# Kernel tuning notes

Measured on AMD Instinct MI355X. Metric: run time of the kernel, lower is better.

The kernel has to match this reference:

```python
import jax, jax.numpy as jnp
import numpy as np
from jax import lax

B, L, D, F = 32, 512, 256, 256
K = 3
EPS = 1e-5


def _layer_norm(h, g, b):
    mu = jnp.mean(h, axis=-1, keepdims=True)
    var = jnp.var(h, axis=-1, keepdims=True)
    return (h - mu) * lax.rsqrt(var + EPS) * g + b


def _conv1d(h, w, b):
    # h: [B, L, Cin], w: [K, Cin, Cout] -> [B, L, Cout], 'same' padding (pad=1, k=3)
    return lax.conv_general_dilated(h, w, window_strides=(1,), padding=[(1, 1)],
                                    dimension_numbers=('NWC', 'WIO', 'NWC')) + b


def _duration_predictor(x, c1w, c1b, ln1g, ln1b, c2w, c2b, ln2g, ln2b, lw, lb):
    h = jax.nn.relu(_layer_norm(_conv1d(x, c1w, c1b), ln1g, ln1b))
    h = jax.nn.relu(_layer_norm(_conv1d(h, c2w, c2b), ln2g, ln2b))
    d = jax.nn.relu(h @ lw + lb)  # [B, L, 1]
    return d[..., 0]              # [B, L] (squeeze, training mode)


def _expand_one(xb, dur, M):
    # xb: [L, D], dur: [L] int. Repeat row i dur[i] times, zero-pad to M frames.
    cs = jnp.cumsum(dur)                              # [L]
    t = jnp.arange(M)                                 # [M]
    idx = jnp.searchsorted(cs, t, side='right')       # phoneme id per frame
    valid = t < cs[-1]
    out = jnp.take(xb, jnp.clip(idx, 0, xb.shape[0] - 1), axis=0)
    return jnp.where(valid[:, None], out, jnp.zeros((), xb.dtype))


def setup_inputs() -> dict:
    key = jax.random.key(0)
    ks = jax.random.split(key, 8)
    s_c = 1.0 / np.sqrt(K * F)
    s_l = 1.0 / np.sqrt(F)
    return {
        'x': jax.random.normal(ks[0], (B, L, D), jnp.float32),
        'durations': jax.random.randint(ks[1], (B, L), 0, 7),
        'mel_max_length': 4096,
        'conv1_w': jax.random.normal(ks[2], (K, D, F), jnp.float32) * s_c,
        'conv1_b': jnp.zeros((F,), jnp.float32),
        'ln1_g': jnp.ones((F,), jnp.float32),
        'ln1_b': jnp.zeros((F,), jnp.float32),
        'conv2_w': jax.random.normal(ks[3], (K, F, F), jnp.float32) * s_c,
        'conv2_b': jnp.zeros((F,), jnp.float32),
        'ln2_g': jnp.ones((F,), jnp.float32),
        'ln2_b': jnp.zeros((F,), jnp.float32),
        'lin_w': jax.random.normal(ks[4], (F, 1), jnp.float32) * s_l,
        'lin_b': jnp.zeros((1,), jnp.float32),
    }


def reference(x, durations, mel_max_length, conv1_w, conv1_b, ln1_g, ln1_b,
              conv2_w, conv2_b, ln2_g, ln2_b, lin_w, lin_b):
    dur_pred = _duration_predictor(x, conv1_w, conv1_b, ln1_g, ln1_b,
                                   conv2_w, conv2_b, ln2_g, ln2_b, lin_w, lin_b)
    dur = durations.astype(jnp.int32)
    output = jax.vmap(lambda xb, db: _expand_one(xb, db, mel_max_length))(x, dur)
    return output, dur_pred
```

## Files before the change

kernel.cpp:

```cpp
#include <hip/hip_runtime.h>

typedef __attribute__((ext_vector_type(8))) short short8;
typedef __attribute__((ext_vector_type(4))) float f32x4;

#define BATCH 32
#define LSEQ  512
#define DIN   256
#define FDIM  256
#define KTOT  768
#define MT    32
#define BK    32

__device__ __forceinline__ short f2bf(float f) {
    union { float f; unsigned u; } v; v.f = f;
    unsigned r = v.u + 0x7FFFu + ((v.u >> 16) & 1u);
    return (short)(r >> 16);
}

__global__ __launch_bounds__(512)
void scan_kernel(const int* __restrict__ dur, int* __restrict__ cs) {
    __shared__ int s[LSEQ];
    const int t = threadIdx.x, b = blockIdx.x;
    s[t] = dur[b * LSEQ + t];
    __syncthreads();
    for (int off = 1; off < LSEQ; off <<= 1) {
        int v = (t >= off) ? s[t - off] : 0;
        __syncthreads();
        s[t] += v;
        __syncthreads();
    }
    cs[b * LSEQ + t] = s[t];
}

__global__ __launch_bounds__(256)
void wprep(const float* __restrict__ w, short* __restrict__ out) {
    const int id = blockIdx.x * 256 + threadIdx.x;
    const int n = id & 255, k = id >> 8;
    out[(((k >> 5) * FDIM) + n) * BK + (k & 31)] = f2bf(w[id]);
}

template<bool AF32, bool FUSE>
__global__ __launch_bounds__(256)
void conv_ln(const void* __restrict__ Asrc, const short* __restrict__ Bt,
             const float* __restrict__ cb, const float* __restrict__ g,
             const float* __restrict__ bta, const float* __restrict__ lw,
             const float* __restrict__ lb, short* __restrict__ Hout,
             float* __restrict__ Dout)
{
    __shared__ short As[MT][BK];
    __shared__ short Bs[FDIM][BK];
    __shared__ float redS[MT][4];
    __shared__ float redQ[MT][4];
    __shared__ float redD[MT][4];
    __shared__ float muS[MT];
    __shared__ float rsS[MT];

    const int tid  = threadIdx.x;
    const int wave = tid >> 6;
    const int lane = tid & 63;
    const int ml   = lane & 15;
    const int q    = lane >> 4;
    const int row0 = blockIdx.x * MT;
    const int bb   = row0 >> 9;

    f32x4 acc[2][4];
    #pragma unroll
    for (int mt = 0; mt < 2; mt++)
        #pragma unroll
        for (int nt = 0; nt < 4; nt++)
            #pragma unroll
            for (int r = 0; r < 4; r++)
                acc[mt][nt][r] = 0.f;

    for (int kc = 0; kc < KTOT; kc += BK) {
        const int tap = kc >> 8;
        const int c0  = kc & 255;
        if (tid < MT * 4) {
            const int r = tid >> 2, part = tid & 3;
            const int l  = (row0 + r) & (LSEQ - 1);
            const int l2 = l + tap - 1;
            short8 v = {0, 0, 0, 0, 0, 0, 0, 0};
            if (l2 >= 0 && l2 < LSEQ) {
                const size_t off = ((size_t)(bb * LSEQ + l2)) * DIN + c0 + part * 8;
                if (AF32) {
                    const float4* s4 = (const float4*)((const float*)Asrc + off);
                    float4 u0 = s4[0], u1 = s4[1];
                    v[0] = f2bf(u0.x); v[1] = f2bf(u0.y); v[2] = f2bf(u0.z); v[3] = f2bf(u0.w);
                    v[4] = f2bf(u1.x); v[5] = f2bf(u1.y); v[6] = f2bf(u1.z); v[7] = f2bf(u1.w);
                } else {
                    v = *(const short8*)((const short*)Asrc + off);
                }
            }
            *(short8*)&As[r][part * 8] = v;
        }
        {
            const short* src = Bt + ((size_t)(kc >> 5) * FDIM + tid) * BK;
            #pragma unroll
            for (int j = 0; j < 4; j++)
                *(short8*)&Bs[tid][j * 8] = *(const short8*)(src + j * 8);
        }
        __syncthreads();
        short8 af[2], bfr[4];
        #pragma unroll
        for (int mt = 0; mt < 2; mt++) af[mt] = *(const short8*)&As[mt * 16 + ml][q * 8];
        #pragma unroll
        for (int nt = 0; nt < 4; nt++) bfr[nt] = *(const short8*)&Bs[wave * 64 + nt * 16 + ml][q * 8];
        #pragma unroll
        for (int mt = 0; mt < 2; mt++)
            #pragma unroll
            for (int nt = 0; nt < 4; nt++)
                acc[mt][nt] = __builtin_amdgcn_mfma_f32_16x16x32_bf16(af[mt], bfr[nt], acc[mt][nt], 0, 0, 0);
        __syncthreads();
    }

    float cbv[4], gv[4], bv[4], lwv[4];
    #pragma unroll
    for (int nt = 0; nt < 4; nt++) {
        const int col = wave * 64 + nt * 16 + ml;
        cbv[nt] = cb[col]; gv[nt] = g[col]; bv[nt] = bta[col];
        lwv[nt] = FUSE ? lw[col] : 0.f;
    }
    #pragma unroll
    for (int mt = 0; mt < 2; mt++)
        #pragma unroll
        for (int nt = 0; nt < 4; nt++)
            #pragma unroll
            for (int r = 0; r < 4; r++)
                acc[mt][nt][r] += cbv[nt];

    #pragma unroll
    for (int mt = 0; mt < 2; mt++)
        #pragma unroll
        for (int r = 0; r < 4; r++) {
            float ps = 0.f, pq = 0.f;
            #pragma unroll
            for (int nt = 0; nt < 4; nt++) { float v = acc[mt][nt][r]; ps += v; pq += v * v; }
            #pragma unroll
            for (int d = 1; d < 16; d <<= 1) { ps += __shfl_xor(ps, d); pq += __shfl_xor(pq, d); }
            if (ml == 0) { const int row = mt * 16 + q * 4 + r; redS[row][wave] = ps; redQ[row][wave] = pq; }
        }
    __syncthreads();
    if (tid < MT) {
        float S = 0.f, Q = 0.f;
        #pragma unroll
        for (int w = 0; w < 4; w++) { S += redS[tid][w]; Q += redQ[tid][w]; }
        const float mu  = S * (1.f / 256.f);
        const float var = Q * (1.f / 256.f) - mu * mu;
        muS[tid] = mu; rsS[tid] = rsqrtf(var + 1e-5f);
    }
    __syncthreads();

    if (!FUSE) {
        #pragma unroll
        for (int mt = 0; mt < 2; mt++)
            #pragma unroll
            for (int r = 0; r < 4; r++) {
                const int row = mt * 16 + q * 4 + r;
                const float mu = muS[row], rs = rsS[row];
                #pragma unroll
                for (int nt = 0; nt < 4; nt++) {
                    const int col = wave * 64 + nt * 16 + ml;
                    float v = (acc[mt][nt][r] - mu) * rs * gv[nt] + bv[nt];
                    v = fmaxf(v, 0.f);
                    Hout[(size_t)(row0 + row) * FDIM + col] = f2bf(v);
                }
            }
    } else {
        #pragma unroll
        for (int mt = 0; mt < 2; mt++)
            #pragma unroll
            for (int r = 0; r < 4; r++) {
                const int row = mt * 16 + q * 4 + r;
                const float mu = muS[row], rs = rsS[row];
                float pd = 0.f;
                #pragma unroll
                for (int nt = 0; nt < 4; nt++) {
                    float v = (acc[mt][nt][r] - mu) * rs * gv[nt] + bv[nt];
                    v = fmaxf(v, 0.f);
                    pd += v * lwv[nt];
                }
                #pragma unroll
                for (int d = 1; d < 16; d <<= 1) pd += __shfl_xor(pd, d);
                if (ml == 0) redD[row][wave] = pd;
            }
        __syncthreads();
        if (tid < MT) {
            float Dv = 0.f;
            #pragma unroll
            for (int w = 0; w < 4; w++) Dv += redD[tid][w];
            Dout[row0 + tid] = fmaxf(Dv + lb[0], 0.f);
        }
    }
}

__global__ __launch_bounds__(256)
void expand_kernel(const float4* __restrict__ x4, const int* __restrict__ cs,
                   float4* __restrict__ out4, int M) {
    const int fr   = blockIdx.x * 4 + (threadIdx.x >> 6);
    const int lane = threadIdx.x & 63;
    const int b = fr / M;
    const int t = fr - b * M;
    const int* csb = cs + b * LSEQ;
    const int total = csb[LSEQ - 1];
    const size_t obase = (size_t)fr * 64 + lane;
    if (t < total) {
        int lo = 0, hi = LSEQ;
        while (lo < hi) { const int mid = (lo + hi) >> 1; if (csb[mid] > t) hi = mid; else lo = mid + 1; }
        const int idx = lo < LSEQ ? lo : LSEQ - 1;
        out4[obase] = x4[((size_t)(b * LSEQ + idx)) * 64 + lane];
    } else {
        out4[obase] = make_float4(0.f, 0.f, 0.f, 0.f);
    }
}

extern "C" void kernel_launch(void* const* d_in, const int* in_sizes, int n_in,
                              void* d_out, int out_size, void* d_ws, size_t ws_size,
                              hipStream_t stream)
{
    const float* x   = (const float*)d_in[0];
    const int*   dur = (const int*)d_in[1];
    const float* c1w = (const float*)d_in[3];
    const float* c1b = (const float*)d_in[4];
    const float* g1  = (const float*)d_in[5];
    const float* b1  = (const float*)d_in[6];
    const float* c2w = (const float*)d_in[7];
    const float* c2b = (const float*)d_in[8];
    const float* g2  = (const float*)d_in[9];
    const float* b2  = (const float*)d_in[10];
    const float* lw  = (const float*)d_in[11];
    const float* lb  = (const float*)d_in[12];

    const int M = (out_size - BATCH * LSEQ) / (BATCH * DIN);
    float* out     = (float*)d_out;
    float* dur_out = out + (size_t)BATCH * M * DIN;

    char* ws   = (char*)d_ws;
    int*   cs  = (int*)ws;
    short* wt1 = (short*)(ws + (64 << 10));
    short* wt2 = (short*)(ws + (64 << 10) + (384 << 10));
    short* h1  = (short*)(ws + (64 << 10) + 2 * (384 << 10));

    hipLaunchKernelGGL(scan_kernel, dim3(BATCH), dim3(LSEQ), 0, stream, dur, cs);
    hipLaunchKernelGGL(wprep, dim3(KTOT), dim3(256), 0, stream, c1w, wt1);
    hipLaunchKernelGGL(wprep, dim3(KTOT), dim3(256), 0, stream, c2w, wt2);
    hipLaunchKernelGGL((conv_ln<true, false>), dim3((BATCH * LSEQ) / MT), dim3(256), 0, stream,
                       (const void*)x, wt1, c1b, g1, b1, (const float*)nullptr, (const float*)nullptr,
                       h1, (float*)nullptr);
    hipLaunchKernelGGL((conv_ln<false, true>), dim3((BATCH * LSEQ) / MT), dim3(256), 0, stream,
                       (const void*)h1, wt2, c2b, g2, b2, lw, lb,
                       (short*)nullptr, dur_out);
    hipLaunchKernelGGL(expand_kernel, dim3((BATCH * M) / 4), dim3(256), 0, stream,
                       (const float4*)x, cs, (float4*)d_out, M);
}
```

Before: 242.8 us.

## Stage full conv input halo in LDS once and stream weights from global

New measurement: 214.9 us. 11.5% less time.

```diff
diff --git a/kernel.cpp b/kernel.cpp
--- a/kernel.cpp
+++ b/kernel.cpp
@@ -10,6 +10,7 @@
 #define KTOT  768
 #define MT    32
 #define BK    32
+#define PADA  264
 
 __device__ __forceinline__ short f2bf(float f) {
     union { float f; unsigned u; } v; v.f = f;
@@ -18,25 +19,28 @@
 }
 
 __global__ __launch_bounds__(512)
-void scan_kernel(const int* __restrict__ dur, int* __restrict__ cs) {
+void prep_kernel(const int* __restrict__ dur, int* __restrict__ cs,
+                 const float* __restrict__ w1, const float* __restrict__ w2,
+                 short* __restrict__ wt1, short* __restrict__ wt2) {
     __shared__ int s[LSEQ];
     const int t = threadIdx.x, b = blockIdx.x;
-    s[t] = dur[b * LSEQ + t];
-    __syncthreads();
-    for (int off = 1; off < LSEQ; off <<= 1) {
-        int v = (t >= off) ? s[t - off] : 0;
+    if (b < BATCH) {
+        s[t] = dur[b * LSEQ + t];
         __syncthreads();
-        s[t] += v;
-        __syncthreads();
-    }
-    cs[b * LSEQ + t] = s[t];
-}
-
-__global__ __launch_bounds__(256)
-void wprep(const float* __restrict__ w, short* __restrict__ out) {
-    const int id = blockIdx.x * 256 + threadIdx.x;
-    const int n = id & 255, k = id >> 8;
-    out[(((k >> 5) * FDIM) + n) * BK + (k & 31)] = f2bf(w[id]);
+        for (int off = 1; off < LSEQ; off <<= 1) {
+            int v = (t >= off) ? s[t - off] : 0;
+            __syncthreads();
+            s[t] += v;
+            __syncthreads();
+        }
+        cs[b * LSEQ + t] = s[t];
+    } else {
+        const int id = (b - BATCH) * 512 + t;
+        const int n = id & 255, k = id >> 8;
+        const int dst = (((k >> 5) * FDIM) + n) * BK + (k & 31);
+        wt1[dst] = f2bf(w1[id]);
+        wt2[dst] = f2bf(w2[id]);
+    }
 }
 
 template<bool AF32, bool FUSE>
@@ -47,8 +51,7 @@
              const float* __restrict__ lb, short* __restrict__ Hout,
              float* __restrict__ Dout)
 {
-    __shared__ short As[MT][BK];
-    __shared__ short Bs[FDIM][BK];
+    __shared__ short As[34][PADA];
     __shared__ float redS[MT][4];
     __shared__ float redQ[MT][4];
     __shared__ float redD[MT][4];
@@ -62,6 +65,26 @@
     const int q    = lane >> 4;
     const int row0 = blockIdx.x * MT;
     const int bb   = row0 >> 9;
+    const int r0   = row0 & (LSEQ - 1);
+
+    for (int idx = tid; idx < 34 * 32; idx += 256) {
+        const int r = idx >> 5, part = idx & 31;
+        const int l2 = r0 + r - 1;
+        short8 v = {0, 0, 0, 0, 0, 0, 0, 0};
+        if (l2 >= 0 && l2 < LSEQ) {
+            const size_t off = ((size_t)(bb * LSEQ + l2)) * DIN + part * 8;
+            if (AF32) {
+                const float4* s4 = (const float4*)((const float*)Asrc + off);
+                float4 u0 = s4[0], u1 = s4[1];
+                v[0] = f2bf(u0.x); v[1] = f2bf(u0.y); v[2] = f2bf(u0.z); v[3] = f2bf(u0.w);
+                v[4] = f2bf(u1.x); v[5] = f2bf(u1.y); v[6] = f2bf(u1.z); v[7] = f2bf(u1.w);
+            } else {
+                v = *(const short8*)((const short*)Asrc + off);
+            }
+        }
+        *(short8*)&As[r][part * 8] = v;
+    }
+    __syncthreads();
 
     f32x4 acc[2][4];
     #pragma unroll
@@ -72,45 +95,27 @@
             for (int r = 0; r < 4; r++)
                 acc[mt][nt][r] = 0.f;
 
-    for (int kc = 0; kc < KTOT; kc += BK) {
-        const int tap = kc >> 8;
-        const int c0  = kc & 255;
-        if (tid < MT * 4) {
-            const int r = tid >> 2, part = tid & 3;
-            const int l  = (row0 + r) & (LSEQ - 1);
-            const int l2 = l + tap - 1;
-            short8 v = {0, 0, 0, 0, 0, 0, 0, 0};
-            if (l2 >= 0 && l2 < LSEQ) {
-                const size_t off = ((size_t)(bb * LSEQ + l2)) * DIN + c0 + part * 8;
-                if (AF32) {
-                    const float4* s4 = (const float4*)((const float*)Asrc + off);
-                    float4 u0 = s4[0], u1 = s4[1];
-                    v[0] = f2bf(u0.x); v[1] = f2bf(u0.y); v[2] = f2bf(u0.z); v[3] = f2bf(u0.w);
-                    v[4] = f2bf(u1.x); v[5] = f2bf(u1.y); v[6] = f2bf(u1.z); v[7] = f2bf(u1.w);
-                } else {
-                    v = *(const short8*)((const short*)Asrc + off);
-                }
-            }
-            *(short8*)&As[r][part * 8] = v;
-        }
-        {
-            const short* src = Bt + ((size_t)(kc >> 5) * FDIM + tid) * BK;
-            #pragma unroll
-            for (int j = 0; j < 4; j++)
-                *(short8*)&Bs[tid][j * 8] = *(const short8*)(src + j * 8);
-        }
-        __syncthreads();
-        short8 af[2], bfr[4];
-        #pragma unroll
-        for (int mt = 0; mt < 2; mt++) af[mt] = *(const short8*)&As[mt * 16 + ml][q * 8];
-        #pragma unroll
-        for (int nt = 0; nt < 4; nt++) bfr[nt] = *(const short8*)&Bs[wave * 64 + nt * 16 + ml][q * 8];
-        #pragma unroll
-        for (int mt = 0; mt < 2; mt++)
-            #pragma unroll
-            for (int nt = 0; nt < 4; nt++)
-                acc[mt][nt] = __builtin_amdgcn_mfma_f32_16x16x32_bf16(af[mt], bfr[nt], acc[mt][nt], 0, 0, 0);
-        __syncthreads();
+    const short* bptr = Bt + (size_t)(wave * 64 + ml) * BK + q * 8;
+    #pragma unroll 1
+    for (int tap = 0; tap < 3; tap++) {
+        #pragma unroll
+        for (int cc = 0; cc < 8; cc++) {
+            short8 af0 = *(const short8*)&As[ml + tap][cc * 32 + q * 8];
+            short8 af1 = *(const short8*)&As[16 + ml + tap][cc * 32 + q * 8];
+            short8 b0 = *(const short8*)(bptr + 0 * 16 * BK);
+            short8 b1 = *(const short8*)(bptr + 1 * 16 * BK);
+            short8 b2 = *(const short8*)(bptr + 2 * 16 * BK);
+            short8 b3 = *(const short8*)(bptr + 3 * 16 * BK);
+            bptr += FDIM * BK;
+            acc[0][0] = __builtin_amdgcn_mfma_f32_16x16x32_bf16(af0, b0, acc[0][0], 0, 0, 0);
+            acc[0][1] = __builtin_amdgcn_mfma_f32_16x16x32_bf16(af0, b1, acc[0][1], 0, 0, 0);
+            acc[0][2] = __builtin_amdgcn_mfma_f32_16x16x32_bf16(af0, b2, acc[0][2], 0, 0, 0);
+            acc[0][3] = __builtin_amdgcn_mfma_f32_16x16x32_bf16(af0, b3, acc[0][3], 0, 0, 0);
+            acc[1][0] = __builtin_amdgcn_mfma_f32_16x16x32_bf16(af1, b0, acc[1][0], 0, 0, 0);
+            acc[1][1] = __builtin_amdgcn_mfma_f32_16x16x32_bf16(af1, b1, acc[1][1], 0, 0, 0);
+            acc[1][2] = __builtin_amdgcn_mfma_f32_16x16x32_bf16(af1, b2, acc[1][2], 0, 0, 0);
+            acc[1][3] = __builtin_amdgcn_mfma_f32_16x16x32_bf16(af1, b3, acc[1][3], 0, 0, 0);
+        }
     }
 
     float cbv[4], gv[4], bv[4], lwv[4];
@@ -240,9 +245,8 @@
     short* wt2 = (short*)(ws + (64 << 10) + (384 << 10));
     short* h1  = (short*)(ws + (64 << 10) + 2 * (384 << 10));
 
-    hipLaunchKernelGGL(scan_kernel, dim3(BATCH), dim3(LSEQ), 0, stream, dur, cs);
-    hipLaunchKernelGGL(wprep, dim3(KTOT), dim3(256), 0, stream, c1w, wt1);
-    hipLaunchKernelGGL(wprep, dim3(KTOT), dim3(256), 0, stream, c2w, wt2);
+    hipLaunchKernelGGL(prep_kernel, dim3(BATCH + (KTOT * FDIM) / 512), dim3(512), 0, stream,
+                       dur, cs, c1w, c2w, wt1, wt2);
     hipLaunchKernelGGL((conv_ln<true, false>), dim3((BATCH * LSEQ) / MT), dim3(256), 0, stream,
                        (const void*)x, wt1, c1b, g1, b1, (const float*)nullptr, (const float*)nullptr,
                        h1, (float*)nullptr);
```
